# Performance work log

Measured on AMD Instinct MI355X. Metric: run time of the kernel, lower is better.

## Reference

```python
import jax, jax.numpy as jnp
import numpy as np

MU = 5
ETA = 1.0
ITERATIONS = 3


def _sobel(x):
    # torch F.conv2d is cross-correlation; replicate exactly
    k = jnp.array([[-1., 0., 1.], [-2., 0., 2.], [-1., 0., 1.]], dtype=x.dtype)
    kernel = jnp.stack([k, k.T])[:, None]  # [2,1,3,3] OIHW
    return jax.lax.conv_general_dilated(
        x, kernel, window_strides=(1, 1), padding=[(1, 1), (1, 1)],
        dimension_numbers=('NCHW', 'OIHW', 'NCHW'))


def _cnorm(v):
    # 2-norm over channel dim, keepdim
    return jnp.sqrt(jnp.sum(v * v, axis=1, keepdims=True))


def setup_inputs() -> dict:
    key = jax.random.key(0)
    inputs = jax.random.uniform(key, (8, 1, 1024, 1024), dtype=jnp.float32)
    return {"inputs": inputs}


def reference(inputs):
    B, _, H, W = inputs.shape
    pad = ((0, 0), (0, 0), (MU, MU), (MU, MU))

    sobel = _sobel(inputs)                       # [B,2,H,W]
    sobel_mag = _cnorm(sobel)                    # [B,1,H,W]
    sobel_mag = sobel_mag / jnp.max(sobel_mag)
    sobel_mag_p = jnp.pad(sobel_mag, pad)

    # tang = flip(sobel, ch) * [-1, 1] -> perpendicular (tangent) field
    tang = jnp.stack([-sobel[:, 1], sobel[:, 0]], axis=1)
    tmag = _cnorm(tang)
    tang = tang / jnp.where(tmag == 0, jnp.ones_like(tmag), tmag)

    for _it in range(ITERATIONS):
        for ori in ('V', 'H'):
            tang_p = jnp.pad(tang, pad)
            tang_X = tang
            acc = jnp.zeros_like(tang)
            for i in range(2 * MU + 1):
                if ori == 'V':
                    tang_Y = tang_p[:, :, i:i + H, MU:MU + W]
                    sob_Y = sobel_mag_p[:, :, i:i + H, MU:MU + W]
                else:
                    tang_Y = tang_p[:, :, MU:MU + H, i:i + W]
                    sob_Y = sobel_mag_p[:, :, MU:MU + H, i:i + W]
                w = (jnp.tanh(ETA * (sob_Y - sobel_mag)) + 1.0) \
                    * jnp.sum(tang_X * tang_Y, axis=1, keepdims=True) * 0.5
                acc = acc + tang_Y * w
            tang = acc
        tmag = _cnorm(tang)
        tang = tang / jnp.where(tmag == 0, jnp.ones_like(tmag), tmag)
    return tang
```

## Files before the change

### kernel.cpp

```cpp
#include <hip/hip_runtime.h>

#define MU 5
static constexpr int Hh = 1024, Ww = 1024, Bb = 8;
static constexpr int NPIX = Bb * Hh * Ww;
static constexpr int TPB = 256;
static constexpr int SOBEL_BLOCKS = NPIX / 4 / TPB;
static constexpr int PY = 8;
static constexpr int PXH = 4;
static constexpr int VBLK = NPIX / PY / TPB;
static constexpr int HBLK = NPIX / PXH / TPB;

__device__ __forceinline__ float rcp_fast(float x) { return __builtin_amdgcn_rcpf(x); }
__device__ __forceinline__ float rsq_fast(float x) { return __builtin_amdgcn_rsqf(x); }

template <int NB>
__device__ __forceinline__ int xcd_swizzle(int bid) {
    return (bid & 7) * (NB / 8) + (bid >> 3);
}

__global__ __launch_bounds__(TPB) void sobel_kernel(
        const float* __restrict__ in, float2* __restrict__ tang,
        float* __restrict__ mag, float* __restrict__ partials) {
    int id = blockIdx.x * TPB + threadIdx.x;
    int xq = id & (Ww / 4 - 1);
    int x0 = xq * 4;
    int y  = (id >> 8) & (Hh - 1);
    int b  = id >> 18;
    const float* p = in + ((size_t)b << 20);

    float c[3][6];
    #pragma unroll
    for (int r = 0; r < 3; ++r) {
        int yy = y - 1 + r;
        bool okr = (yy >= 0) && (yy < Hh);
        const float* row = p + (okr ? yy : 0) * Ww;
        float4 v = okr ? *(const float4*)(row + x0) : make_float4(0.f, 0.f, 0.f, 0.f);
        c[r][1] = v.x; c[r][2] = v.y; c[r][3] = v.z; c[r][4] = v.w;
        c[r][0] = (okr && x0 > 0)      ? row[x0 - 1] : 0.0f;
        c[r][5] = (okr && x0 + 4 < Ww) ? row[x0 + 4] : 0.0f;
    }

    float S[6], D[6];
    #pragma unroll
    for (int cc = 0; cc < 6; ++cc) {
        S[cc] = c[0][cc] + 2.0f * c[1][cc] + c[2][cc];
        D[cc] = c[2][cc] - c[0][cc];
    }

    float2 tg[4];
    float  mg[4];
    float vmax = 0.0f;
    #pragma unroll
    for (int k = 0; k < 4; ++k) {
        float gx = S[k + 2] - S[k];
        float gy = D[k] + 2.0f * D[k + 1] + D[k + 2];
        float g2 = gx * gx + gy * gy;
        float irs = rsq_fast(g2);
        float m   = (g2 > 0.0f) ? g2 * irs : 0.0f;
        float inv = (g2 > 0.0f) ? irs : 1.0f;
        mg[k] = m;
        tg[k] = make_float2(-gy * inv, gx * inv);
        vmax = fmaxf(vmax, m);
    }

    int idx = (b << 20) + y * Ww + x0;
    *(float4*)&mag[idx] = make_float4(mg[0], mg[1], mg[2], mg[3]);
    float4* tp = (float4*)&tang[idx];
    tp[0] = make_float4(tg[0].x, tg[0].y, tg[1].x, tg[1].y);
    tp[1] = make_float4(tg[2].x, tg[2].y, tg[3].x, tg[3].y);

    #pragma unroll
    for (int off = 32; off; off >>= 1) vmax = fmaxf(vmax, __shfl_xor(vmax, off));
    __shared__ float smax[4];
    int lane = threadIdx.x & 63, wid = threadIdx.x >> 6;
    if (lane == 0) smax[wid] = vmax;
    __syncthreads();
    if (threadIdx.x == 0)
        partials[blockIdx.x] = fmaxf(fmaxf(smax[0], smax[1]), fmaxf(smax[2], smax[3]));
}

__global__ void max_reduce_kernel(const float* __restrict__ partials,
                                  float* __restrict__ scale_out) {
    float v = 0.0f;
    for (int i = threadIdx.x; i < SOBEL_BLOCKS; i += 1024)
        v = fmaxf(v, partials[i]);
    #pragma unroll
    for (int off = 32; off; off >>= 1) v = fmaxf(v, __shfl_xor(v, off));
    __shared__ float smax[16];
    int lane = threadIdx.x & 63, wid = threadIdx.x >> 6;
    if (lane == 0) smax[wid] = v;
    __syncthreads();
    if (threadIdx.x == 0) {
        float m = smax[0];
        #pragma unroll
        for (int i = 1; i < 16; ++i) m = fmaxf(m, smax[i]);
        *scale_out = 1.0f / m;
    }
}

__global__ void prep_kernel(float4* __restrict__ mag4,
                            const float* __restrict__ scalep) {
    int id = blockIdx.x * blockDim.x + threadIdx.x;
    float k = 2.0f * (*scalep);
    float4 m = mag4[id];
    m.x = __expf(k * m.x);
    m.y = __expf(k * m.y);
    m.z = __expf(k * m.z);
    m.w = __expf(k * m.w);
    mag4[id] = m;
}

__global__ __launch_bounds__(TPB) void etf_v(const float2* __restrict__ src,
                                             float2* __restrict__ dst,
                                             const float* __restrict__ E) {
    int bid = xcd_swizzle<VBLK>((int)blockIdx.x);
    int gid = bid * TPB + threadIdx.x;
    int x = gid & (Ww - 1);
    int yg = (gid >> 10) & (Hh / PY - 1);
    int b = gid >> 17;
    int y0 = yg * PY;
    int base = b << 20;

    float2 t[PY + 10];
    float  e[PY + 10];
    if (yg >= 1 && yg <= Hh / PY - 2) {
        #pragma unroll
        for (int r = 0; r < PY + 10; ++r) {
            int j = base + (y0 - MU + r) * Ww + x;
            t[r] = src[j];
            e[r] = E[j];
        }
    } else {
        #pragma unroll
        for (int r = 0; r < PY + 10; ++r) {
            int row = y0 - MU + r;
            bool ok = (row >= 0) && (row < Hh);
            int j = base + (ok ? row : 0) * Ww + x;
            t[r] = ok ? src[j] : make_float2(0.0f, 0.0f);
            e[r] = ok ? E[j] : 1.0f;
        }
    }

    #pragma unroll
    for (int k = 0; k < PY; ++k) {
        float2 tX = t[k + MU];
        float  eX = e[k + MU];
        float ax = 0.0f, ay = 0.0f;
        #pragma unroll
        for (int i = 0; i <= 2 * MU; ++i) {
            float2 tY = t[k + i];
            float  eY = e[k + i];
            float d = tX.x * tY.x + tX.y * tY.y;
            float w = eY * rcp_fast(eX + eY) * d;
            ax += tY.x * w;
            ay += tY.y * w;
        }
        dst[base + (y0 + k) * Ww + x] = make_float2(ax, ay);
    }
}

template <bool FINAL>
__global__ __launch_bounds__(TPB) void etf_h(const float2* __restrict__ src,
                                             float2* __restrict__ dstI,
                                             float* __restrict__ dstP,
                                             const float* __restrict__ E) {
    int bid = xcd_swizzle<HBLK>((int)blockIdx.x);
    int gid = bid * TPB + threadIdx.x;
    int xq = gid & (Ww / PXH - 1);
    int x0 = xq * PXH;
    int y = (gid >> 8) & (Hh - 1);
    int b = gid >> 18;
    int rowbase = (b << 20) + y * Ww;

    float2 t[PXH + 10];
    float  e[PXH + 10];
    if (xq >= 2 && xq <= Ww / PXH - 3) {
        #pragma unroll
        for (int r = 0; r < PXH + 10; ++r) {
            int j = rowbase + x0 - MU + r;
            t[r] = src[j];
            e[r] = E[j];
        }
    } else {
        #pragma unroll
        for (int r = 0; r < PXH + 10; ++r) {
            int col = x0 - MU + r;
            bool ok = (col >= 0) && (col < Ww);
            int j = rowbase + (ok ? col : 0);
            t[r] = ok ? src[j] : make_float2(0.0f, 0.0f);
            e[r] = ok ? E[j] : 1.0f;
        }
    }

    float ox[PXH], oy[PXH];
    #pragma unroll
    for (int k = 0; k < PXH; ++k) {
        float2 tX = t[k + MU];
        float  eX = e[k + MU];
        float ax = 0.0f, ay = 0.0f;
        #pragma unroll
        for (int i = 0; i <= 2 * MU; ++i) {
            float2 tY = t[k + i];
            float  eY = e[k + i];
            float d = tX.x * tY.x + tX.y * tY.y;
            float w = eY * rcp_fast(eX + eY) * d;
            ax += tY.x * w;
            ay += tY.y * w;
        }
        float n2 = ax * ax + ay * ay;
        float inv = (n2 > 0.0f) ? rsq_fast(n2) : 1.0f;
        ox[k] = ax * inv;
        oy[k] = ay * inv;
    }

    if (FINAL) {
        *(float4*)&dstP[((size_t)(b * 2 + 0) << 20) + y * Ww + x0] =
            make_float4(ox[0], ox[1], ox[2], ox[3]);
        *(float4*)&dstP[((size_t)(b * 2 + 1) << 20) + y * Ww + x0] =
            make_float4(oy[0], oy[1], oy[2], oy[3]);
    } else {
        float4* dp = (float4*)&dstI[rowbase + x0];
        dp[0] = make_float4(ox[0], oy[0], ox[1], oy[1]);
        dp[1] = make_float4(ox[2], oy[2], ox[3], oy[3]);
    }
}

extern "C" void kernel_launch(void* const* d_in, const int* in_sizes, int n_in,
                              void* d_out, int out_size, void* d_ws, size_t ws_size,
                              hipStream_t stream) {
    const float* in = (const float*)d_in[0];
    float* out = (float*)d_out;
    char* ws = (char*)d_ws;

    float* magE = (float*)ws;
    float2* tA = (float2*)(ws + (size_t)NPIX * sizeof(float));
    float* partials = (float*)(ws + (size_t)NPIX * sizeof(float)
                                  + (size_t)NPIX * sizeof(float2));
    float* scalep = partials + SOBEL_BLOCKS;
    float2* tOut = (float2*)out;

    sobel_kernel<<<SOBEL_BLOCKS, TPB, 0, stream>>>(in, tOut, magE, partials);
    max_reduce_kernel<<<1, 1024, 0, stream>>>(partials, scalep);
    prep_kernel<<<NPIX / 4 / TPB, TPB, 0, stream>>>((float4*)magE, scalep);

    etf_v<<<VBLK, TPB, 0, stream>>>(tOut, tA, magE);
    etf_h<false><<<HBLK, TPB, 0, stream>>>(tA, tOut, nullptr, magE);
    etf_v<<<VBLK, TPB, 0, stream>>>(tOut, tA, magE);
    etf_h<false><<<HBLK, TPB, 0, stream>>>(tA, tOut, nullptr, magE);
    etf_v<<<VBLK, TPB, 0, stream>>>(tOut, tA, magE);
    etf_h<true ><<<HBLK, TPB, 0, stream>>>(tA, nullptr, out, magE);
}
```

Before: 234.1 us.

## Recompute Sobel in two passes to fuse exp prep, and double vertical rows per thread

Splits the Sobel stage into a max-only pass that writes nothing but partial maxima of squared gradient, then a second pass that recomputes Sobel and writes the tangent field and exp-weights directly. This removes the separate prep kernel's read-modify-write of the magnitude buffer at the cost of re-reading the input image. The vertical flow kernel now processes 16 rows per thread instead of 8, cutting halo reloads but raising register use.

```diff
diff --git a/kernel.cpp b/kernel.cpp
--- a/kernel.cpp
+++ b/kernel.cpp
@@ -5,7 +5,7 @@
 static constexpr int NPIX = Bb * Hh * Ww;
 static constexpr int TPB = 256;
 static constexpr int SOBEL_BLOCKS = NPIX / 4 / TPB;
-static constexpr int PY = 8;
+static constexpr int PY = 16;
 static constexpr int PXH = 4;
 static constexpr int VBLK = NPIX / PY / TPB;
 static constexpr int HBLK = NPIX / PXH / TPB;
@@ -18,16 +18,9 @@
     return (bid & 7) * (NB / 8) + (bid >> 3);
 }
 
-__global__ __launch_bounds__(TPB) void sobel_kernel(
-        const float* __restrict__ in, float2* __restrict__ tang,
-        float* __restrict__ mag, float* __restrict__ partials) {
-    int id = blockIdx.x * TPB + threadIdx.x;
-    int xq = id & (Ww / 4 - 1);
-    int x0 = xq * 4;
-    int y  = (id >> 8) & (Hh - 1);
-    int b  = id >> 18;
-    const float* p = in + ((size_t)b << 20);
-
+__device__ __forceinline__ void sobel4(const float* __restrict__ p,
+                                       int y, int x0,
+                                       float gx[4], float gy[4]) {
     float c[3][6];
     #pragma unroll
     for (int r = 0; r < 3; ++r) {
@@ -39,35 +32,35 @@
         c[r][0] = (okr && x0 > 0)      ? row[x0 - 1] : 0.0f;
         c[r][5] = (okr && x0 + 4 < Ww) ? row[x0 + 4] : 0.0f;
     }
-
     float S[6], D[6];
     #pragma unroll
     for (int cc = 0; cc < 6; ++cc) {
         S[cc] = c[0][cc] + 2.0f * c[1][cc] + c[2][cc];
         D[cc] = c[2][cc] - c[0][cc];
     }
-
-    float2 tg[4];
-    float  mg[4];
+    #pragma unroll
+    for (int k = 0; k < 4; ++k) {
+        gx[k] = S[k + 2] - S[k];
+        gy[k] = D[k] + 2.0f * D[k + 1] + D[k + 2];
+    }
+}
+
+__global__ __launch_bounds__(TPB) void maxg2_kernel(
+        const float* __restrict__ in, float* __restrict__ partials) {
+    int id = blockIdx.x * TPB + threadIdx.x;
+    int xq = id & (Ww / 4 - 1);
+    int x0 = xq * 4;
+    int y  = (id >> 8) & (Hh - 1);
+    int b  = id >> 18;
+    const float* p = in + ((size_t)b << 20);
+
+    float gx[4], gy[4];
+    sobel4(p, y, x0, gx, gy);
+
     float vmax = 0.0f;
     #pragma unroll
-    for (int k = 0; k < 4; ++k) {
-        float gx = S[k + 2] - S[k];
-        float gy = D[k] + 2.0f * D[k + 1] + D[k + 2];
-        float g2 = gx * gx + gy * gy;
-        float irs = rsq_fast(g2);
-        float m   = (g2 > 0.0f) ? g2 * irs : 0.0f;
-        float inv = (g2 > 0.0f) ? irs : 1.0f;
-        mg[k] = m;
-        tg[k] = make_float2(-gy * inv, gx * inv);
-        vmax = fmaxf(vmax, m);
-    }
-
-    int idx = (b << 20) + y * Ww + x0;
-    *(float4*)&mag[idx] = make_float4(mg[0], mg[1], mg[2], mg[3]);
-    float4* tp = (float4*)&tang[idx];
-    tp[0] = make_float4(tg[0].x, tg[0].y, tg[1].x, tg[1].y);
-    tp[1] = make_float4(tg[2].x, tg[2].y, tg[3].x, tg[3].y);
+    for (int k = 0; k < 4; ++k)
+        vmax = fmaxf(vmax, gx[k] * gx[k] + gy[k] * gy[k]);
 
     #pragma unroll
     for (int off = 32; off; off >>= 1) vmax = fmaxf(vmax, __shfl_xor(vmax, off));
@@ -94,20 +87,41 @@
         float m = smax[0];
         #pragma unroll
         for (int i = 1; i < 16; ++i) m = fmaxf(m, smax[i]);
-        *scale_out = 1.0f / m;
-    }
-}
-
-__global__ void prep_kernel(float4* __restrict__ mag4,
-                            const float* __restrict__ scalep) {
-    int id = blockIdx.x * blockDim.x + threadIdx.x;
-    float k = 2.0f * (*scalep);
-    float4 m = mag4[id];
-    m.x = __expf(k * m.x);
-    m.y = __expf(k * m.y);
-    m.z = __expf(k * m.z);
-    m.w = __expf(k * m.w);
-    mag4[id] = m;
+        *scale_out = 1.0f / sqrtf(m);
+    }
+}
+
+__global__ __launch_bounds__(TPB) void sobelE_kernel(
+        const float* __restrict__ in, float2* __restrict__ tang,
+        float* __restrict__ E, const float* __restrict__ scalep) {
+    int id = blockIdx.x * TPB + threadIdx.x;
+    int xq = id & (Ww / 4 - 1);
+    int x0 = xq * 4;
+    int y  = (id >> 8) & (Hh - 1);
+    int b  = id >> 18;
+    const float* p = in + ((size_t)b << 20);
+    float k2 = 2.0f * (*scalep);
+
+    float gx[4], gy[4];
+    sobel4(p, y, x0, gx, gy);
+
+    float2 tg[4];
+    float  eg[4];
+    #pragma unroll
+    for (int k = 0; k < 4; ++k) {
+        float g2 = gx[k] * gx[k] + gy[k] * gy[k];
+        float irs = rsq_fast(g2);
+        float m   = (g2 > 0.0f) ? g2 * irs : 0.0f;
+        float inv = (g2 > 0.0f) ? irs : 1.0f;
+        tg[k] = make_float2(-gy[k] * inv, gx[k] * inv);
+        eg[k] = __expf(k2 * m);
+    }
+
+    int idx = (b << 20) + y * Ww + x0;
+    *(float4*)&E[idx] = make_float4(eg[0], eg[1], eg[2], eg[3]);
+    float4* tp = (float4*)&tang[idx];
+    tp[0] = make_float4(tg[0].x, tg[0].y, tg[1].x, tg[1].y);
+    tp[1] = make_float4(tg[2].x, tg[2].y, tg[3].x, tg[3].y);
 }
 
 __global__ __launch_bounds__(TPB) void etf_v(const float2* __restrict__ src,
@@ -117,7 +131,7 @@
     int gid = bid * TPB + threadIdx.x;
     int x = gid & (Ww - 1);
     int yg = (gid >> 10) & (Hh / PY - 1);
-    int b = gid >> 17;
+    int b = gid >> 16;
     int y0 = yg * PY;
     int base = b << 20;
 
@@ -239,9 +253,9 @@
     float* scalep = partials + SOBEL_BLOCKS;
     float2* tOut = (float2*)out;
 
-    sobel_kernel<<<SOBEL_BLOCKS, TPB, 0, stream>>>(in, tOut, magE, partials);
+    maxg2_kernel<<<SOBEL_BLOCKS, TPB, 0, stream>>>(in, partials);
     max_reduce_kernel<<<1, 1024, 0, stream>>>(partials, scalep);
-    prep_kernel<<<NPIX / 4 / TPB, TPB, 0, stream>>>((float4*)magE, scalep);
+    sobelE_kernel<<<SOBEL_BLOCKS, TPB, 0, stream>>>(in, tOut, magE, scalep);
 
     etf_v<<<VBLK, TPB, 0, stream>>>(tOut, tA, magE);
     etf_h<false><<<HBLK, TPB, 0, stream>>>(tA, tOut, nullptr, magE);
```

Result: no change. 234.2 us (+0.0%).
